# Optimization experiments

Measured on AMD Instinct MI355X. Metric: run time of the kernel, lower is better.

## Reference

```python
import jax, jax.numpy as jnp
import numpy as np

B, N, D, H = 2, 2048, 128, 128  # batch, n_nodes, node_dim, hidden_dim
HQ = H // 4
EPS_DIST = 1e-8
EPS_LN = 1e-5


def setup_inputs() -> dict:
    key = jax.random.key(0)
    ks = jax.random.split(key, 12)
    s = 0.02
    return {
        "h": jax.random.normal(ks[0], (B, N, D), jnp.float32),
        "coords": jax.random.uniform(ks[1], (B, N, 2), jnp.float32),
        "Wq": jax.random.normal(ks[2], (D, H), jnp.float32) * s,
        "bq": jnp.zeros((H,), jnp.float32),
        "Wk": jax.random.normal(ks[3], (D, H), jnp.float32) * s,
        "bk": jnp.zeros((H,), jnp.float32),
        "Wv": jax.random.normal(ks[4], (D, H), jnp.float32) * s,
        "bv": jnp.zeros((H,), jnp.float32),
        "Wd1": jax.random.normal(ks[5], (1, HQ), jnp.float32) * s,
        "bd1": jnp.zeros((HQ,), jnp.float32),
        "Wd2": jax.random.normal(ks[6], (HQ, 1), jnp.float32) * s,
        "bd2": jnp.zeros((1,), jnp.float32),
        "Wo": jax.random.normal(ks[7], (H, D), jnp.float32) * s,
        "bo": jnp.zeros((D,), jnp.float32),
        "gamma": jnp.ones((D,), jnp.float32),
        "beta": jnp.zeros((D,), jnp.float32),
    }


def reference(h, coords, Wq, bq, Wk, bk, Wv, bv, Wd1, bd1, Wd2, bd2, Wo, bo, gamma, beta):
    q = h @ Wq + bq                      # (B, N, H)
    k = h @ Wk + bk
    v = h @ Wv + bv
    scores = jnp.einsum('bnh,bmh->bnm', q, k) / jnp.sqrt(jnp.float32(H))  # (B,N,N)
    # pairwise Euclidean distances
    diff = coords[:, :, None, :] - coords[:, None, :, :]                  # (B,N,N,2)
    dist = jnp.sqrt(jnp.sum(diff * diff, axis=-1, keepdims=True) + EPS_DIST)  # (B,N,N,1)
    hmid = jax.nn.silu(dist @ Wd1 + bd1)                                  # (B,N,N,HQ)
    dist_bias = (hmid @ Wd2 + bd2)[..., 0]                                # (B,N,N)
    attn = jax.nn.softmax(scores + dist_bias, axis=-1)
    out = jnp.einsum('bnm,bmh->bnh', attn, v)                             # (B,N,H)
    out = jax.nn.silu(out @ Wo + bo)                                      # (B,N,D)
    res = h + out
    mu = jnp.mean(res, axis=-1, keepdims=True)
    var = jnp.mean((res - mu) ** 2, axis=-1, keepdims=True)
    return (res - mu) / jnp.sqrt(var + EPS_LN) * gamma + beta
```

## Files before the change

### kernel.cpp

```cpp
#include <hip/hip_runtime.h>
#include <hip/hip_bf16.h>

#define B_ 2
#define N_ 2048
#define D_ 128
#define H_ 128
#define HQ_ 32
#define ROWS_ (B_*N_)
#define KS_ 16
#define KPP_ (N_/KS_)
#define DMAX_ 1.4143f
#define SCALE_ 0.08838834764831845f
#define LOG2E_ 1.4426950408889634f

typedef __bf16 bf16x4 __attribute__((ext_vector_type(4)));
typedef __bf16 bf16x8 __attribute__((ext_vector_type(8)));
typedef float  f32x4  __attribute__((ext_vector_type(4)));
typedef unsigned short ushort8 __attribute__((ext_vector_type(8)));

#if __has_builtin(__builtin_amdgcn_exp2f)
#define EXP2F_ __builtin_amdgcn_exp2f
#else
#define EXP2F_ exp2f
#endif
#if __has_builtin(__builtin_amdgcn_sqrtf)
#define SQRTF_ __builtin_amdgcn_sqrtf
#else
#define SQRTF_ sqrtf
#endif

#define Q_OFF    0
#define K_OFF    (ROWS_*H_*2)
#define V_OFF    (2*ROWS_*H_*2)
#define L_OFF    (3*ROWS_*H_*2)
#define OP_OFF   (L_OFF + ROWS_*KS_*4)
#define HB_OFF   (OP_OFF + (size_t)ROWS_*KS_*H_*2)
#define WT_OFF   (HB_OFF + ROWS_*D_*2)
#define CF_OFF   (WT_OFF + 3*D_*H_*2)

__global__ __launch_bounds__(256) void prep_kernel(
    const float* __restrict__ h,
    const float* __restrict__ Wq, const float* __restrict__ Wk, const float* __restrict__ Wv,
    const float* __restrict__ Wd1, const float* __restrict__ bd1,
    const float* __restrict__ Wd2, const float* __restrict__ bd2,
    __bf16* __restrict__ hb, __bf16* __restrict__ Wt, float* __restrict__ cf)
{
    const int bid = blockIdx.x, t = threadIdx.x;
    if (bid < 256) {
        const float4* src = (const float4*)(h + (size_t)bid * 2048);
        __bf16* dst = hb + (size_t)bid * 2048;
        #pragma unroll
        for (int i = 0; i < 2; ++i) {
            float4 v = src[t + i * 256];
            bf16x4 pk = { (__bf16)v.x, (__bf16)v.y, (__bf16)v.z, (__bf16)v.w };
            *(bf16x4*)(dst + (t + i * 256) * 4) = pk;
        }
    } else if (bid < 280) {
        __shared__ float tile[128][17];
        const int id = bid - 256;
        const int m = id >> 3, ch = id & 7;
        const float* W = m == 0 ? Wq : (m == 1 ? Wk : Wv);
        const int c0 = ch * 16;
        #pragma unroll
        for (int i = 0; i < 8; ++i) {
            int idx = t + i * 256;
            int k = idx >> 4, cc = idx & 15;
            tile[k][cc] = W[k * 128 + c0 + cc];
        }
        __syncthreads();
        __bf16* dst = Wt + m * 16384;
        #pragma unroll
        for (int i = 0; i < 8; ++i) {
            int idx = t + i * 256;
            int cc = idx >> 7, k = idx & 127;
            dst[(c0 + cc) * 128 + k] = (__bf16)tile[k][cc];
        }
    } else if (t < 64) {
        const int j = t & 31;
        const float w1 = Wd1[j], b1 = bd1[j];
        const float w2h = Wd2[j] * 0.5f;
        float gv[5];
        #pragma unroll
        for (int i = 0; i < 5; ++i) {
            float d = (DMAX_ * 0.25f) * (float)i;
            float x = fmaf(d, w1, b1);
            gv[i] = (x / (1.f + __expf(-x))) * w2h;
        }
        #pragma unroll
        for (int i = 0; i < 5; ++i)
            #pragma unroll
            for (int off = 1; off < 64; off <<= 1) gv[i] += __shfl_xor(gv[i], off);
        if (t == 0) {
            const float bd2v = bd2[0];
            float g0 = (gv[0] + bd2v) * LOG2E_, g1 = (gv[1] + bd2v) * LOG2E_,
                  g2 = (gv[2] + bd2v) * LOG2E_, g3 = (gv[3] + bd2v) * LOG2E_,
                  g4 = (gv[4] + bd2v) * LOG2E_;
            cf[0] = g0;
            cf[1] = -2.0833333333f*g0 + 4.f*g1 - 3.f*g2 + 1.3333333333f*g3 - 0.25f*g4;
            cf[2] =  1.4583333333f*g0 - 4.3333333333f*g1 + 4.75f*g2 - 2.3333333333f*g3 + 0.4583333333f*g4;
            cf[3] = -0.4166666667f*g0 + 1.5f*g1 - 2.f*g2 + 1.1666666667f*g3 - 0.25f*g4;
            cf[4] =  0.0416666667f*g0 - 0.1666666667f*g1 + 0.25f*g2 - 0.1666666667f*g3 + 0.0416666667f*g4;
        }
    }
}

__global__ __launch_bounds__(256) void qkv_mfma(
    const __bf16* __restrict__ hb, const __bf16* __restrict__ Wt,
    const float* __restrict__ bq, const float* __restrict__ bk, const float* __restrict__ bv,
    __bf16* __restrict__ qb, __bf16* __restrict__ kb, __bf16* __restrict__ vb)
{
    const int t = threadIdx.x, wid = t >> 6, lane = t & 63;
    const int l16 = lane & 15, g = lane >> 4;
    const int row0 = blockIdx.x * 64 + wid * 16;
    const int co   = blockIdx.y * 32;
    const int which = co >> 7, c0 = co & 127;
    const __bf16* Wm = Wt + which * 16384;
    __bf16* outp      = which == 0 ? qb : (which == 1 ? kb : vb);
    const float* bias = which == 0 ? bq : (which == 1 ? bk : bv);
    const float scale = which == 0 ? (SCALE_ * LOG2E_) : 1.f;

    bf16x8 af[4];
    const __bf16* arow = hb + (size_t)(row0 + l16) * 128;
    #pragma unroll
    for (int kk = 0; kk < 4; ++kk) af[kk] = *(const bf16x8*)(arow + kk * 32 + g * 8);

    f32x4 acc0 = {0.f,0.f,0.f,0.f}, acc1 = {0.f,0.f,0.f,0.f};
    const __bf16* b0 = Wm + (size_t)(c0 + l16) * 128;
    const __bf16* b1 = Wm + (size_t)(c0 + 16 + l16) * 128;
    #pragma unroll
    for (int kk = 0; kk < 4; ++kk) {
        bf16x8 f0 = *(const bf16x8*)(b0 + kk * 32 + g * 8);
        acc0 = __builtin_amdgcn_mfma_f32_16x16x32_bf16(af[kk], f0, acc0, 0, 0, 0);
    }
    #pragma unroll
    for (int kk = 0; kk < 4; ++kk) {
        bf16x8 f1 = *(const bf16x8*)(b1 + kk * 32 + g * 8);
        acc1 = __builtin_amdgcn_mfma_f32_16x16x32_bf16(af[kk], f1, acc1, 0, 0, 0);
    }
    const float bv0 = bias[c0 + l16], bv1 = bias[c0 + 16 + l16];
    #pragma unroll
    for (int i = 0; i < 4; ++i) {
        size_t r = (size_t)(row0 + g * 4 + i) * 128;
        outp[r + c0 + l16]      = (__bf16)((acc0[i] + bv0) * scale);
        outp[r + c0 + 16 + l16] = (__bf16)((acc1[i] + bv1) * scale);
    }
}

__global__ __launch_bounds__(256, 4) void attn_kernel(
    const __bf16* __restrict__ qb, const __bf16* __restrict__ kb, const __bf16* __restrict__ vb,
    const float* __restrict__ coords, const float* __restrict__ cfp,
    unsigned int* __restrict__ Opb32, float* __restrict__ Larr)
{
    __shared__ __align__(16) unsigned int Vsu[2][128][20];
    __shared__ __align__(16) __bf16 Pl[4][16][40];

    const int t    = threadIdx.x;
    const int wid  = t >> 6;
    const int lane = t & 63;
    const int l16  = lane & 15;
    const int g    = lane >> 4;
    const int qbase = blockIdx.x * 64 + wid * 16;
    const int p     = blockIdx.y;
    const int b     = qbase >> 11;

    const float c0 = cfp[0], c1 = cfp[1], c2 = cfp[2], c3 = cfp[3], c4 = cfp[4];

    bf16x8 qf[4];
    const __bf16* qrow = qb + (size_t)(qbase + l16) * H_;
    #pragma unroll
    for (int kk = 0; kk < 4; ++kk) qf[kk] = *(const bf16x8*)(qrow + kk * 32 + g * 8);

    float cx[4], cy[4];
    #pragma unroll
    for (int i = 0; i < 4; ++i) {
        int qr = qbase + g * 4 + i;
        cx[i] = coords[qr * 2]; cy[i] = coords[qr * 2 + 1];
    }

    float l_i[4] = {0.f, 0.f, 0.f, 0.f};
    f32x4 O[8];
    #pragma unroll
    for (int c = 0; c < 8; ++c) O[c] = (f32x4){0.f, 0.f, 0.f, 0.f};

    const int kp = t & 15, co = t >> 4;
    const int kgbase = (b << 11) + p * KPP_;
    const int NT = KPP_ / 32;

    {
        const __bf16* sp = vb + (size_t)(kgbase + 2 * kp) * H_ + co * 8;
        bf16x8 va = *(const bf16x8*)sp;
        bf16x8 vb2 = *(const bf16x8*)(sp + H_);
        ushort8 ua = __builtin_bit_cast(ushort8, va);
        ushort8 ub = __builtin_bit_cast(ushort8, vb2);
        #pragma unroll
        for (int j = 0; j < 8; ++j)
            Vsu[0][co * 8 + j][kp] = (unsigned)ua[j] | ((unsigned)ub[j] << 16);
    }

    for (int kt = 0; kt < NT; ++kt) {
        __syncthreads();

        bf16x8 nva, nvb;
        if (kt + 1 < NT) {
            const __bf16* sp = vb + (size_t)(kgbase + (kt + 1) * 32 + 2 * kp) * H_ + co * 8;
            nva = *(const bf16x8*)sp;
            nvb = *(const bf16x8*)(sp + H_);
        }

        const int kg = kgbase + kt * 32;
        #pragma unroll
        for (int mt = 0; mt < 2; ++mt) {
            f32x4 acc = (f32x4){0.f, 0.f, 0.f, 0.f};
            const __bf16* krow = kb + (size_t)(kg + mt * 16 + l16) * H_;
            #pragma unroll
            for (int kk = 0; kk < 4; ++kk) {
                bf16x8 kf = *(const bf16x8*)(krow + kk * 32 + g * 8);
                acc = __builtin_amdgcn_mfma_f32_16x16x32_bf16(qf[kk], kf, acc, 0, 0, 0);
            }
            float2 kc = *(const float2*)&coords[(kg + mt * 16 + l16) * 2];
            #pragma unroll
            for (int i = 0; i < 4; ++i) {
                float dx = cx[i] - kc.x, dy = cy[i] - kc.y;
                float dist = SQRTF_(fmaf(dx, dx, fmaf(dy, dy, 1e-8f)));
                float s4 = dist * (4.0f / DMAX_);
                float bias = fmaf(fmaf(fmaf(fmaf(c4, s4, c3), s4, c2), s4, c1), s4, c0);
                float sc = fminf(acc[i] + bias, 80.f);
                float pe = EXP2F_(sc);
                l_i[i] += pe;
                Pl[wid][g * 4 + i][mt * 16 + l16] = (__bf16)pe;
            }
        }

        if (kt + 1 < NT) {
            ushort8 ua = __builtin_bit_cast(ushort8, nva);
            ushort8 ub = __builtin_bit_cast(ushort8, nvb);
            #pragma unroll
            for (int j = 0; j < 8; ++j)
                Vsu[(kt + 1) & 1][co * 8 + j][kp] = (unsigned)ua[j] | ((unsigned)ub[j] << 16);
        }

        bf16x8 pf = *(const bf16x8*)&Pl[wid][l16][g * 8];
        #pragma unroll
        for (int c = 0; c < 8; ++c) {
            bf16x8 vf = *(const bf16x8*)&Vsu[kt & 1][c * 16 + l16][g * 4];
            O[c] = __builtin_amdgcn_mfma_f32_16x16x32_bf16(pf, vf, O[c], 0, 0, 0);
        }
    }

    const size_t rpbase = (size_t)p * (ROWS_ / 2) + (qbase >> 1) + g * 2;
    #pragma unroll
    for (int c = 0; c < 8; ++c)
        #pragma unroll
        for (int ip = 0; ip < 2; ++ip) {
            unsigned lo = __builtin_bit_cast(unsigned, O[c][2 * ip]);
            unsigned hi = __builtin_bit_cast(unsigned, O[c][2 * ip + 1]);
            Opb32[(rpbase + ip) * H_ + c * 16 + l16] = (hi & 0xffff0000u) | (lo >> 16);
        }

    #pragma unroll
    for (int i = 0; i < 4; ++i) {
        float lv = l_i[i];
        lv += __shfl_xor(lv, 1); lv += __shfl_xor(lv, 2);
        lv += __shfl_xor(lv, 4); lv += __shfl_xor(lv, 8);
        if (l16 == 0) Larr[(qbase + g * 4 + i) * KS_ + p] = lv;
    }
}

__global__ __launch_bounds__(256) void final_kernel(
    const unsigned int* __restrict__ Opb32, const float* __restrict__ Larr,
    const float* __restrict__ h, const float* __restrict__ Wo, const float* __restrict__ bo,
    const float* __restrict__ gamma, const float* __restrict__ beta, float* __restrict__ out)
{
    __shared__ __align__(16) float as_[8][128];
    __shared__ float redS[4][4], redQ[4][4];
    const int t = threadIdx.x;
    const int c = t & 127;
    const int rh = t >> 7;
    const int bx = blockIdx.x;
    const int row0 = (bx & 63) * 64 + (bx >> 6) * 8;

    #pragma unroll
    for (int pr = 0; pr < 2; ++pr) {
        int r0 = rh * 4 + pr * 2;
        int row = row0 + r0;
        size_t rp = (size_t)row >> 1;
        float accL = 0.f, accH = 0.f, lsumL = 0.f, lsumH = 0.f;
        #pragma unroll
        for (int p = 0; p < KS_; ++p) {
            unsigned v = Opb32[((size_t)p * (ROWS_ / 2) + rp) * H_ + c];
            accL += __uint_as_float(v << 16);
            accH += __uint_as_float(v & 0xffff0000u);
        }
        #pragma unroll
        for (int q4 = 0; q4 < 4; ++q4) {
            f32x4 lL = *(const f32x4*)&Larr[row * KS_ + q4 * 4];
            f32x4 lH = *(const f32x4*)&Larr[(row + 1) * KS_ + q4 * 4];
            lsumL += lL[0] + lL[1] + lL[2] + lL[3];
            lsumH += lH[0] + lH[1] + lH[2] + lH[3];
        }
        as_[r0][c]     = accL / lsumL;
        as_[r0 + 1][c] = accH / lsumH;
    }
    __syncthreads();

    float acc4[4] = {0.f, 0.f, 0.f, 0.f};
    #pragma unroll 4
    for (int d4 = 0; d4 < 32; ++d4) {
        float w0 = Wo[(d4 * 4 + 0) * 128 + c];
        float w1 = Wo[(d4 * 4 + 1) * 128 + c];
        float w2 = Wo[(d4 * 4 + 2) * 128 + c];
        float w3 = Wo[(d4 * 4 + 3) * 128 + c];
        #pragma unroll
        for (int r = 0; r < 4; ++r) {
            f32x4 a_ = *(const f32x4*)&as_[rh * 4 + r][d4 * 4];
            acc4[r] = fmaf(a_[0], w0, acc4[r]);
            acc4[r] = fmaf(a_[1], w1, acc4[r]);
            acc4[r] = fmaf(a_[2], w2, acc4[r]);
            acc4[r] = fmaf(a_[3], w3, acc4[r]);
        }
    }

    const float bov = bo[c], gv = gamma[c], bvv = beta[c];
    const int wv = t >> 6;
    float res[4];
    #pragma unroll
    for (int r = 0; r < 4; ++r) {
        float x = acc4[r] + bov;
        float sl = x / (1.f + __expf(-x));
        res[r] = h[(size_t)(row0 + rh * 4 + r) * 128 + c] + sl;
    }

    #pragma unroll
    for (int r = 0; r < 4; ++r) {
        float s1 = res[r], s2 = res[r] * res[r];
        #pragma unroll
        for (int off = 32; off >= 1; off >>= 1) {
            s1 += __shfl_xor(s1, off);
            s2 += __shfl_xor(s2, off);
        }
        if ((t & 63) == 0) { redS[wv][r] = s1; redQ[wv][r] = s2; }
    }
    __syncthreads();
    #pragma unroll
    for (int r = 0; r < 4; ++r) {
        float sum = redS[2 * rh][r] + redS[2 * rh + 1][r];
        float sq  = redQ[2 * rh][r] + redQ[2 * rh + 1][r];
        float mu  = sum * (1.f / 128.f);
        float var = sq * (1.f / 128.f) - mu * mu;
        out[(size_t)(row0 + rh * 4 + r) * 128 + c] = (res[r] - mu) * rsqrtf(var + 1e-5f) * gv + bvv;
    }
}

extern "C" void kernel_launch(void* const* d_in, const int* in_sizes, int n_in,
                              void* d_out, int out_size, void* d_ws, size_t ws_size,
                              hipStream_t stream)
{
    const float* h      = (const float*)d_in[0];
    const float* coords = (const float*)d_in[1];
    const float* Wq = (const float*)d_in[2];  const float* bq = (const float*)d_in[3];
    const float* Wk = (const float*)d_in[4];  const float* bk = (const float*)d_in[5];
    const float* Wv = (const float*)d_in[6];  const float* bv = (const float*)d_in[7];
    const float* Wd1 = (const float*)d_in[8]; const float* bd1 = (const float*)d_in[9];
    const float* Wd2 = (const float*)d_in[10];const float* bd2 = (const float*)d_in[11];
    const float* Wo = (const float*)d_in[12]; const float* bo = (const float*)d_in[13];
    const float* gamma = (const float*)d_in[14]; const float* beta = (const float*)d_in[15];

    char* ws = (char*)d_ws;
    __bf16* qb = (__bf16*)(ws + Q_OFF);
    __bf16* kb = (__bf16*)(ws + K_OFF);
    __bf16* vb = (__bf16*)(ws + V_OFF);
    float* Larr         = (float*)(ws + L_OFF);
    unsigned int* Opb32 = (unsigned int*)(ws + OP_OFF);
    __bf16* hb   = (__bf16*)(ws + HB_OFF);
    __bf16* Wt   = (__bf16*)(ws + WT_OFF);
    float* cf    = (float*)(ws + CF_OFF);

    prep_kernel<<<281, 256, 0, stream>>>(h, Wq, Wk, Wv, Wd1, bd1, Wd2, bd2, hb, Wt, cf);
    qkv_mfma<<<dim3(ROWS_ / 64, 12), 256, 0, stream>>>(hb, Wt, bq, bk, bv, qb, kb, vb);
    attn_kernel<<<dim3(ROWS_ / 64, KS_), 256, 0, stream>>>(qb, kb, vb, coords, cf, Opb32, Larr);
    final_kernel<<<ROWS_ / 8, 256, 0, stream>>>(Opb32, Larr, h, Wo, bo, gamma, beta, (float*)d_out);
}
```

Baseline: 53.81 us.

## Process two query tiles per wave in attention to reuse K and V loads

Each wave now handles two 16-row query tiles (128 queries per block instead of 64), so every K fragment loaded from global memory and every V tile staged in shared memory feeds twice as many MFMAs. The grid is halved and final_kernel's row mapping is updated to match. This cuts K/V traffic and staging overhead per unit of work, but doubles accumulator registers, which lowers the occupancy target to 3 blocks per CU and halves the number of blocks.

```diff
diff --git a/kernel.cpp b/kernel.cpp
--- a/kernel.cpp
+++ b/kernel.cpp
@@ -146,41 +146,46 @@
     }
 }
 
-__global__ __launch_bounds__(256, 4) void attn_kernel(
+__global__ __launch_bounds__(256, 3) void attn_kernel(
     const __bf16* __restrict__ qb, const __bf16* __restrict__ kb, const __bf16* __restrict__ vb,
     const float* __restrict__ coords, const float* __restrict__ cfp,
     unsigned int* __restrict__ Opb32, float* __restrict__ Larr)
 {
     __shared__ __align__(16) unsigned int Vsu[2][128][20];
-    __shared__ __align__(16) __bf16 Pl[4][16][40];
+    __shared__ __align__(16) __bf16 Pl[4][2][16][40];
 
     const int t    = threadIdx.x;
     const int wid  = t >> 6;
     const int lane = t & 63;
     const int l16  = lane & 15;
     const int g    = lane >> 4;
-    const int qbase = blockIdx.x * 64 + wid * 16;
-    const int p     = blockIdx.y;
-    const int b     = qbase >> 11;
+    const int qb0  = blockIdx.x * 128 + wid * 16;
+    const int p    = blockIdx.y;
+    const int b    = blockIdx.x >> 4;
 
     const float c0 = cfp[0], c1 = cfp[1], c2 = cfp[2], c3 = cfp[3], c4 = cfp[4];
 
-    bf16x8 qf[4];
-    const __bf16* qrow = qb + (size_t)(qbase + l16) * H_;
-    #pragma unroll
-    for (int kk = 0; kk < 4; ++kk) qf[kk] = *(const bf16x8*)(qrow + kk * 32 + g * 8);
-
-    float cx[4], cy[4];
-    #pragma unroll
-    for (int i = 0; i < 4; ++i) {
-        int qr = qbase + g * 4 + i;
-        cx[i] = coords[qr * 2]; cy[i] = coords[qr * 2 + 1];
-    }
-
-    float l_i[4] = {0.f, 0.f, 0.f, 0.f};
-    f32x4 O[8];
-    #pragma unroll
-    for (int c = 0; c < 8; ++c) O[c] = (f32x4){0.f, 0.f, 0.f, 0.f};
+    bf16x8 qf[2][4];
+    #pragma unroll
+    for (int tt = 0; tt < 2; ++tt) {
+        const __bf16* qrow = qb + (size_t)(qb0 + tt * 64 + l16) * H_;
+        #pragma unroll
+        for (int kk = 0; kk < 4; ++kk) qf[tt][kk] = *(const bf16x8*)(qrow + kk * 32 + g * 8);
+    }
+
+    float cx[2][4], cy[2][4];
+    #pragma unroll
+    for (int tt = 0; tt < 2; ++tt)
+        #pragma unroll
+        for (int i = 0; i < 4; ++i) {
+            int qr = qb0 + tt * 64 + g * 4 + i;
+            cx[tt][i] = coords[qr * 2]; cy[tt][i] = coords[qr * 2 + 1];
+        }
+
+    float l_i[2][4] = {{0.f,0.f,0.f,0.f},{0.f,0.f,0.f,0.f}};
+    f32x4 O0[8], O1[8];
+    #pragma unroll
+    for (int c = 0; c < 8; ++c) { O0[c] = (f32x4){0.f,0.f,0.f,0.f}; O1[c] = (f32x4){0.f,0.f,0.f,0.f}; }
 
     const int kp = t & 15, co = t >> 4;
     const int kgbase = (b << 11) + p * KPP_;
@@ -210,24 +215,41 @@
         const int kg = kgbase + kt * 32;
         #pragma unroll
         for (int mt = 0; mt < 2; ++mt) {
-            f32x4 acc = (f32x4){0.f, 0.f, 0.f, 0.f};
+            bf16x8 kf[4];
             const __bf16* krow = kb + (size_t)(kg + mt * 16 + l16) * H_;
             #pragma unroll
-            for (int kk = 0; kk < 4; ++kk) {
-                bf16x8 kf = *(const bf16x8*)(krow + kk * 32 + g * 8);
-                acc = __builtin_amdgcn_mfma_f32_16x16x32_bf16(qf[kk], kf, acc, 0, 0, 0);
-            }
+            for (int kk = 0; kk < 4; ++kk) kf[kk] = *(const bf16x8*)(krow + kk * 32 + g * 8);
+
+            f32x4 acc0 = {0.f,0.f,0.f,0.f}, acc1 = {0.f,0.f,0.f,0.f};
+            #pragma unroll
+            for (int kk = 0; kk < 4; ++kk)
+                acc0 = __builtin_amdgcn_mfma_f32_16x16x32_bf16(qf[0][kk], kf[kk], acc0, 0, 0, 0);
+            #pragma unroll
+            for (int kk = 0; kk < 4; ++kk)
+                acc1 = __builtin_amdgcn_mfma_f32_16x16x32_bf16(qf[1][kk], kf[kk], acc1, 0, 0, 0);
+
             float2 kc = *(const float2*)&coords[(kg + mt * 16 + l16) * 2];
             #pragma unroll
             for (int i = 0; i < 4; ++i) {
-                float dx = cx[i] - kc.x, dy = cy[i] - kc.y;
+                float dx = cx[0][i] - kc.x, dy = cy[0][i] - kc.y;
                 float dist = SQRTF_(fmaf(dx, dx, fmaf(dy, dy, 1e-8f)));
                 float s4 = dist * (4.0f / DMAX_);
                 float bias = fmaf(fmaf(fmaf(fmaf(c4, s4, c3), s4, c2), s4, c1), s4, c0);
-                float sc = fminf(acc[i] + bias, 80.f);
+                float sc = fminf(acc0[i] + bias, 80.f);
                 float pe = EXP2F_(sc);
-                l_i[i] += pe;
-                Pl[wid][g * 4 + i][mt * 16 + l16] = (__bf16)pe;
+                l_i[0][i] += pe;
+                Pl[wid][0][g * 4 + i][mt * 16 + l16] = (__bf16)pe;
+            }
+            #pragma unroll
+            for (int i = 0; i < 4; ++i) {
+                float dx = cx[1][i] - kc.x, dy = cy[1][i] - kc.y;
+                float dist = SQRTF_(fmaf(dx, dx, fmaf(dy, dy, 1e-8f)));
+                float s4 = dist * (4.0f / DMAX_);
+                float bias = fmaf(fmaf(fmaf(fmaf(c4, s4, c3), s4, c2), s4, c1), s4, c0);
+                float sc = fminf(acc1[i] + bias, 80.f);
+                float pe = EXP2F_(sc);
+                l_i[1][i] += pe;
+                Pl[wid][1][g * 4 + i][mt * 16 + l16] = (__bf16)pe;
             }
         }
 
@@ -239,31 +261,40 @@
                 Vsu[(kt + 1) & 1][co * 8 + j][kp] = (unsigned)ua[j] | ((unsigned)ub[j] << 16);
         }
 
-        bf16x8 pf = *(const bf16x8*)&Pl[wid][l16][g * 8];
+        bf16x8 pf0 = *(const bf16x8*)&Pl[wid][0][l16][g * 8];
+        bf16x8 pf1 = *(const bf16x8*)&Pl[wid][1][l16][g * 8];
         #pragma unroll
         for (int c = 0; c < 8; ++c) {
             bf16x8 vf = *(const bf16x8*)&Vsu[kt & 1][c * 16 + l16][g * 4];
-            O[c] = __builtin_amdgcn_mfma_f32_16x16x32_bf16(pf, vf, O[c], 0, 0, 0);
-        }
-    }
-
-    const size_t rpbase = (size_t)p * (ROWS_ / 2) + (qbase >> 1) + g * 2;
-    #pragma unroll
-    for (int c = 0; c < 8; ++c)
-        #pragma unroll
-        for (int ip = 0; ip < 2; ++ip) {
-            unsigned lo = __builtin_bit_cast(unsigned, O[c][2 * ip]);
-            unsigned hi = __builtin_bit_cast(unsigned, O[c][2 * ip + 1]);
-            Opb32[(rpbase + ip) * H_ + c * 16 + l16] = (hi & 0xffff0000u) | (lo >> 16);
-        }
-
-    #pragma unroll
-    for (int i = 0; i < 4; ++i) {
-        float lv = l_i[i];
-        lv += __shfl_xor(lv, 1); lv += __shfl_xor(lv, 2);
-        lv += __shfl_xor(lv, 4); lv += __shfl_xor(lv, 8);
-        if (l16 == 0) Larr[(qbase + g * 4 + i) * KS_ + p] = lv;
-    }
+            O0[c] = __builtin_amdgcn_mfma_f32_16x16x32_bf16(pf0, vf, O0[c], 0, 0, 0);
+            O1[c] = __builtin_amdgcn_mfma_f32_16x16x32_bf16(pf1, vf, O1[c], 0, 0, 0);
+        }
+    }
+
+    #pragma unroll
+    for (int tt = 0; tt < 2; ++tt) {
+        const size_t rpbase = (size_t)p * (ROWS_ / 2) + ((qb0 + tt * 64) >> 1) + g * 2;
+        #pragma unroll
+        for (int c = 0; c < 8; ++c)
+            #pragma unroll
+            for (int ip = 0; ip < 2; ++ip) {
+                float lo_f = tt ? O1[c][2 * ip]     : O0[c][2 * ip];
+                float hi_f = tt ? O1[c][2 * ip + 1] : O0[c][2 * ip + 1];
+                unsigned lo = __builtin_bit_cast(unsigned, lo_f);
+                unsigned hi = __builtin_bit_cast(unsigned, hi_f);
+                Opb32[(rpbase + ip) * H_ + c * 16 + l16] = (hi & 0xffff0000u) | (lo >> 16);
+            }
+    }
+
+    #pragma unroll
+    for (int tt = 0; tt < 2; ++tt)
+        #pragma unroll
+        for (int i = 0; i < 4; ++i) {
+            float lv = l_i[tt][i];
+            lv += __shfl_xor(lv, 1); lv += __shfl_xor(lv, 2);
+            lv += __shfl_xor(lv, 4); lv += __shfl_xor(lv, 8);
+            if (l16 == 0) Larr[(qb0 + tt * 64 + g * 4 + i) * KS_ + p] = lv;
+        }
 }
 
 __global__ __launch_bounds__(256) void final_kernel(
@@ -277,7 +308,7 @@
     const int c = t & 127;
     const int rh = t >> 7;
     const int bx = blockIdx.x;
-    const int row0 = (bx & 63) * 64 + (bx >> 6) * 8;
+    const int row0 = (bx & 31) * 128 + (bx >> 5) * 8;
 
     #pragma unroll
     for (int pr = 0; pr < 2; ++pr) {
@@ -377,6 +408,6 @@
 
     prep_kernel<<<281, 256, 0, stream>>>(h, Wq, Wk, Wv, Wd1, bd1, Wd2, bd2, hb, Wt, cf);
     qkv_mfma<<<dim3(ROWS_ / 64, 12), 256, 0, stream>>>(hb, Wt, bq, bk, bv, qb, kb, vb);
-    attn_kernel<<<dim3(ROWS_ / 64, KS_), 256, 0, stream>>>(qb, kb, vb, coords, cf, Opb32, Larr);
+    attn_kernel<<<dim3(ROWS_ / 128, KS_), 256, 0, stream>>>(qb, kb, vb, coords, cf, Opb32, Larr);
     final_kernel<<<ROWS_ / 8, 256, 0, stream>>>(Opb32, Larr, h, Wo, bo, gamma, beta, (float*)d_out);
 }
```

Measured after the change: 50.14 us. 1.07x faster.
